# Kernel tuning notes

Hardware: AMD Instinct MI355X
Metric: run time of the kernel (lower is better)

## Reference

```python
import jax, jax.numpy as jnp
import numpy as np

B, S, D, E, K = 4, 2048, 1024, 8, 2
EPS, W_THRES, TEMP = 1e-4, 0.1, 1.0


def setup_inputs() -> dict:
    key = jax.random.key(0)
    k1, k2, k3, k4, k5 = jax.random.split(key, 5)
    x = jax.random.normal(k1, (B, S, D), dtype=jnp.float32)
    gate_W = jax.random.normal(k2, (D, E), dtype=jnp.float32) * 0.02
    gate_b = jnp.zeros((E,), dtype=jnp.float32)
    expert_W = jax.random.normal(k3, (E, D, D), dtype=jnp.float32) * 0.02
    expert_b = jnp.zeros((E, D), dtype=jnp.float32)
    return {"x": x, "gate_W": gate_W, "gate_b": gate_b,
            "expert_W": expert_W, "expert_b": expert_b}


def reference(x, gate_W, gate_b, expert_W, expert_b):
    # Gating: linear -> temperature -> clamp-min(eps) -> softmax
    scores = jnp.maximum((x @ gate_W + gate_b) / TEMP, EPS)      # [B,S,E]
    p = jax.nn.softmax(scores, axis=-1)                           # [B,S,E]
    _, topk_idx = jax.lax.top_k(p, K)                             # [B,S,K]
    # boolean membership mask of selected experts
    topk_mask = jax.nn.one_hot(topk_idx, E, dtype=p.dtype).sum(-2) > 0  # [B,S,E]
    # weights: clamp-min(weight_thres), normalized by detached sum over selected
    w = jnp.maximum(p, W_THRES)                                   # [B,S,E]
    w_gather = jnp.take_along_axis(w, topk_idx, axis=-1)          # [B,S,K]
    total = jax.lax.stop_gradient(w_gather.sum(-1, keepdims=True))
    w = w / total
    comb = jnp.where(topk_mask, w, jnp.zeros_like(w))             # [B,S,E]
    # Dense equivalent of gather/expert/scatter loop (E small): each expert
    # is Linear(D, D); masked combine weights zero out unselected experts.
    y = jnp.einsum('bsd,edf->bsef', x, expert_W) + expert_b       # [B,S,E,D]
    out = jnp.einsum('bsef,bse->bsf', y, comb) / K                # [B,S,D]
    return out
```

## Files before the change

kernel.cpp:

```cpp
#include <hip/hip_runtime.h>
#include <stdint.h>

#define TOK 8192
#define DIM 1024
#define NE 8
#define NTILE 136

typedef short bf16x8 __attribute__((ext_vector_type(8)));
typedef float f32x4 __attribute__((ext_vector_type(4)));

__device__ __forceinline__ unsigned short f2bf(float f) {
  unsigned int u = __float_as_uint(f);
  u += 0x7FFFu + ((u >> 16) & 1u);
  return (unsigned short)(u >> 16);
}

__device__ __forceinline__ void gl_lds16(const void* g, void* l) {
  __builtin_amdgcn_global_load_lds(
      (__attribute__((address_space(1))) unsigned int*)(g),
      (__attribute__((address_space(3))) unsigned int*)(l), 16, 0, 0);
}

__global__ __launch_bounds__(256) void gate_kernel(
    const float* __restrict__ x, const float* __restrict__ gW,
    const float* __restrict__ gb, unsigned short* __restrict__ xb,
    int* __restrict__ eSel, float* __restrict__ wSel, int* __restrict__ cnt)
{
  if (blockIdx.x == 0 && threadIdx.x < NE) cnt[threadIdx.x] = 0;

  const int wave = threadIdx.x >> 6;
  const int lane = threadIdx.x & 63;
  const int t = blockIdx.x * 4 + wave;
  const float4* xrow = (const float4*)(x + (size_t)t * DIM);
  ushort4* xbrow = (ushort4*)(xb + (size_t)t * DIM);

  double acc[NE];
#pragma unroll
  for (int e = 0; e < NE; ++e) acc[e] = 0.0;

#pragma unroll
  for (int i = 0; i < 4; ++i) {
    const int j = i * 64 + lane;
    float4 v = xrow[j];
    ushort4 pk;
    pk.x = f2bf(v.x); pk.y = f2bf(v.y); pk.z = f2bf(v.z); pk.w = f2bf(v.w);
    xbrow[j] = pk;
    const float* g = gW + (size_t)j * 4 * NE;
    float xv[4] = {v.x, v.y, v.z, v.w};
#pragma unroll
    for (int c = 0; c < 4; ++c) {
#pragma unroll
      for (int e = 0; e < NE; ++e)
        acc[e] += (double)xv[c] * (double)g[c * NE + e];
    }
  }
#pragma unroll
  for (int off = 32; off > 0; off >>= 1) {
#pragma unroll
    for (int e = 0; e < NE; ++e)
      acc[e] += __shfl_xor(acc[e], off, 64);
  }

  if (lane == 0) {
    double s[NE];
#pragma unroll
    for (int e = 0; e < NE; ++e) {
      s[e] = acc[e] + (double)gb[e];
      if (s[e] < 1e-4) s[e] = 1e-4;
    }
    int e0 = 0;
    for (int e = 1; e < NE; ++e) if (s[e] > s[e0]) e0 = e;
    int e1 = (e0 == 0) ? 1 : 0;
    for (int e = 0; e < NE; ++e) if (e != e0 && s[e] > s[e1]) e1 = e;
    float m = (float)s[e0];
    float Z = 0.f, pf[NE];
#pragma unroll
    for (int e = 0; e < NE; ++e) { pf[e] = __expf((float)s[e] - m); Z += pf[e]; }
    float w0 = pf[e0] / Z; if (w0 < 0.1f) w0 = 0.1f;
    float w1 = pf[e1] / Z; if (w1 < 0.1f) w1 = 0.1f;
    const float inv = 0.5f / (w0 + w1);
    eSel[t * 2 + 0] = e0;
    eSel[t * 2 + 1] = e1;
    wSel[t * 2 + 0] = w0 * inv;
    wSel[t * 2 + 1] = w1 * inv;
  }
}

__global__ __launch_bounds__(256) void scatter_kernel(
    const int* __restrict__ eSel, const float* __restrict__ wSel,
    int* __restrict__ cnt, int* __restrict__ listTok, float* __restrict__ listW)
{
  __shared__ int lcnt[NE];
  __shared__ int base[NE];
  const int tid = threadIdx.x;
  if (tid < NE) lcnt[tid] = 0;
  __syncthreads();

  const int t = blockIdx.x * 256 + tid;
  const int e0 = eSel[t * 2 + 0];
  const int e1 = eSel[t * 2 + 1];
  const float w0 = wSel[t * 2 + 0];
  const float w1 = wSel[t * 2 + 1];
  const int l0 = atomicAdd(&lcnt[e0], 1);
  const int l1 = atomicAdd(&lcnt[e1], 1);
  __syncthreads();
  if (tid < NE) base[tid] = atomicAdd(&cnt[tid], lcnt[tid]);
  __syncthreads();

  const int p0 = base[e0] + l0;
  listTok[e0 * TOK + p0] = t * 2 + 0;
  listW [e0 * TOK + p0] = w0;
  const int p1 = base[e1] + l1;
  listTok[e1 * TOK + p1] = t * 2 + 1;
  listW [e1 * TOK + p1] = w1;
}

__global__ __launch_bounds__(256) void transpose_w(
    const float* __restrict__ W, unsigned short* __restrict__ Wt)
{
  __shared__ float t[32 * 17 + 16];
  const int e  = blockIdx.x >> 6;
  const int fb = blockIdx.x & 63;
  const int f0 = fb * 16;
  const int tid = threadIdx.x;
  const float* Wb = W + (size_t)e * DIM * DIM + f0;
  unsigned short* Ob = Wt + ((size_t)(e * 64 + fb) * 32) * 512;

  for (int kc = 0; kc < 32; ++kc) {
    const int d0 = kc * 32;
    __syncthreads();
#pragma unroll
    for (int h = 0; h < 512; h += 256) {
      const int idx = tid + h;
      t[(idx >> 4) * 17 + (idx & 15)] = Wb[(size_t)(d0 + (idx >> 4)) * DIM + (idx & 15)];
    }
    __syncthreads();
#pragma unroll
    for (int h = 0; h < 512; h += 256) {
      const int o = tid + h;
      Ob[(size_t)kc * 512 + o] = f2bf(t[(o & 31) * 17 + (o >> 5)]);
    }
  }
}

__global__ __launch_bounds__(256) void moe_gemm(
    const unsigned short* __restrict__ xb, const unsigned short* __restrict__ Wt,
    const float* __restrict__ eb, const int* __restrict__ cnt,
    const int* __restrict__ listTok, const float* __restrict__ listW,
    float* __restrict__ yslot)
{
  const int dId = blockIdx.x % NTILE;
  const int cT  = blockIdx.x / NTILE;
  int e = -1, r0 = 0, rows = 0, accT = 0;
#pragma unroll
  for (int ee = 0; ee < NE; ++ee) {
    const int c = cnt[ee];
    const int nt = (c + 127) >> 7;
    if (dId >= accT && dId < accT + nt) {
      e = ee; r0 = (dId - accT) * 128;
      rows = c - r0; if (rows > 128) rows = 128;
    }
    accT += nt;
  }
  if (e < 0) return;

  __shared__ __align__(16) unsigned short As[2][128 * 32];
  __shared__ int   tid_s[128];
  __shared__ float w_s[128];

  const int tid = threadIdx.x;
  if (tid < 128) {
    if (tid < rows) {
      tid_s[tid] = listTok[e * TOK + r0 + tid];
      w_s[tid]   = listW [e * TOK + r0 + tid];
    } else {
      tid_s[tid] = 0;
      w_s[tid]   = 0.0f;
    }
  }
  __syncthreads();

  const int w    = tid >> 6;
  const int lane = tid & 63;
  const int qsrc = (lane & 3) ^ ((lane >> 3) & 3);
  const int rA0  = w * 32 + (lane >> 2);
  const int rA1  = rA0 + 16;
  const unsigned short* srcA0 = xb + (size_t)(tid_s[rA0] >> 1) * DIM + qsrc * 8;
  const unsigned short* srcA1 = xb + (size_t)(tid_s[rA1] >> 1) * DIM + qsrc * 8;

  const int wr = w >> 1, wc = w & 1;
  const int mrow = lane & 15;
  const int qg   = lane >> 4;
  const int qsA  = (qg ^ ((mrow >> 1) & 3)) * 8;

  const unsigned short* bbase =
      Wt + ((size_t)(e * 64 + cT * 8 + wc * 4) * 32) * 512 + mrow * 32 + qg * 8;

  f32x4 acc[4][4];
#pragma unroll
  for (int i = 0; i < 4; ++i)
#pragma unroll
    for (int j = 0; j < 4; ++j)
      acc[i][j] = {0.f, 0.f, 0.f, 0.f};

  gl_lds16(srcA0, &As[0][w * 1024]);
  gl_lds16(srcA1, &As[0][w * 1024 + 512]);

  for (int kc = 0; kc < DIM / 32; ++kc) {
    const int cur = kc & 1;
    __syncthreads();
    bf16x8 b[4];
#pragma unroll
    for (int nt = 0; nt < 4; ++nt)
      b[nt] = *(const bf16x8*)(bbase + (size_t)nt * 16384 + kc * 512);
    if (kc < DIM / 32 - 1) {
      const int k1 = (kc + 1) * 32;
      unsigned short* a = &As[cur ^ 1][w * 1024];
      gl_lds16(srcA0 + k1, a);
      gl_lds16(srcA1 + k1, a + 512);
    }
    bf16x8 af[4];
#pragma unroll
    for (int mt = 0; mt < 4; ++mt)
      af[mt] = *(const bf16x8*)&As[cur][(wr * 64 + mt * 16 + mrow) * 32 + qsA];
#pragma unroll
    for (int nt = 0; nt < 4; ++nt)
#pragma unroll
      for (int mt = 0; mt < 4; ++mt)
        acc[mt][nt] = __builtin_amdgcn_mfma_f32_16x16x32_bf16(
            af[mt], b[nt], acc[mt][nt], 0, 0, 0);
  }

  const int colBase = cT * 128 + wc * 64 + mrow;
  float bias[4];
#pragma unroll
  for (int nt = 0; nt < 4; ++nt)
    bias[nt] = eb[(size_t)e * DIM + colBase + nt * 16];
#pragma unroll
  for (int mt = 0; mt < 4; ++mt) {
#pragma unroll
    for (int r = 0; r < 4; ++r) {
      const int rloc = wr * 64 + mt * 16 + (lane >> 4) * 4 + r;
      if (rloc < rows) {
        const int tk    = tid_s[rloc];
        const float wgt = w_s[rloc];
        float* dst = yslot + ((size_t)(tk & 1) * TOK + (size_t)(tk >> 1)) * DIM;
#pragma unroll
        for (int nt = 0; nt < 4; ++nt)
          dst[colBase + nt * 16] = wgt * (acc[mt][nt][r] + bias[nt]);
      }
    }
  }
}

__global__ __launch_bounds__(256) void combine(
    const float4* __restrict__ y0, const float4* __restrict__ y1,
    float4* __restrict__ out)
{
  const size_t i = (size_t)blockIdx.x * 256 + threadIdx.x;
  float4 a = y0[i], b = y1[i];
  float4 o;
  o.x = a.x + b.x; o.y = a.y + b.y; o.z = a.z + b.z; o.w = a.w + b.w;
  out[i] = o;
}

extern "C" void kernel_launch(void* const* d_in, const int* in_sizes, int n_in,
                              void* d_out, int out_size, void* d_ws, size_t ws_size,
                              hipStream_t stream)
{
  const float* x  = (const float*)d_in[0];
  const float* gW = (const float*)d_in[1];
  const float* gb = (const float*)d_in[2];
  const float* eW = (const float*)d_in[3];
  const float* eb = (const float*)d_in[4];
  float* out = (float*)d_out;

  char* p = (char*)d_ws;
  unsigned short* xb = (unsigned short*)p;  p += (size_t)TOK * DIM * 2;
  unsigned short* Wt = (unsigned short*)p;  p += (size_t)NE * DIM * DIM * 2;
  float* yslot = (float*)p;                 p += (size_t)2 * TOK * DIM * 4;
  int* cnt = (int*)p;                       p += 256;
  int* listTok = (int*)p;                   p += (size_t)NE * TOK * 4;
  float* listW = (float*)p;                 p += (size_t)NE * TOK * 4;

  int*   eSel = (int*)yslot;
  float* wSel = (float*)(yslot + TOK * 2);

  gate_kernel<<<TOK / 4, 256, 0, stream>>>(x, gW, gb, xb, eSel, wSel, cnt);
  scatter_kernel<<<TOK / 256, 256, 0, stream>>>(eSel, wSel, cnt, listTok, listW);
  transpose_w<<<NE * 64, 256, 0, stream>>>(eW, Wt);
  moe_gemm<<<NTILE * 8, 256, 0, stream>>>(xb, Wt, eb, cnt, listTok, listW, yslot);
  combine<<<TOK * DIM / 4 / 256, 256, 0, stream>>>(
      (const float4*)yslot, (const float4*)yslot + (size_t)TOK * DIM / 4, (float4*)out);
}
```

Before: 233.2 us.

## Stage gate weights in LDS, stage B tiles via LDS, store expert outputs in fp16

The gate kernel now copies the gate weights into shared memory once per block in an expert-major layout, replacing the strided global loads in its dot products. The expert weight transpose now writes a plain row-major [f][d] bf16 layout. The GEMM streams B tiles into double-buffered LDS with async global-to-LDS loads, the same way it already handles A, instead of loading B fragments straight from global memory per step. Per-slot expert outputs are written as fp16, which halves the intermediate write and read traffic in the combine step but adds rounding error and extra LDS use per block.

```diff
diff --git a/kernel.cpp b/kernel.cpp
--- a/kernel.cpp
+++ b/kernel.cpp
@@ -1,4 +1,5 @@
 #include <hip/hip_runtime.h>
+#include <hip/hip_fp16.h>
 #include <stdint.h>
 
 #define TOK 8192
@@ -27,6 +28,19 @@
     int* __restrict__ eSel, float* __restrict__ wSel, int* __restrict__ cnt)
 {
   if (blockIdx.x == 0 && threadIdx.x < NE) cnt[threadIdx.x] = 0;
+
+  __shared__ float gWs[NE * DIM];
+#pragma unroll
+  for (int h = 0; h < 8; ++h) {
+    const int m = threadIdx.x + h * 256;
+    float4 v = ((const float4*)gW)[m];
+    const int d = m >> 1, e0 = (m & 1) * 4;
+    gWs[(e0 + 0) * DIM + d] = v.x;
+    gWs[(e0 + 1) * DIM + d] = v.y;
+    gWs[(e0 + 2) * DIM + d] = v.z;
+    gWs[(e0 + 3) * DIM + d] = v.w;
+  }
+  __syncthreads();
 
   const int wave = threadIdx.x >> 6;
   const int lane = threadIdx.x & 63;
@@ -45,13 +59,11 @@
     ushort4 pk;
     pk.x = f2bf(v.x); pk.y = f2bf(v.y); pk.z = f2bf(v.z); pk.w = f2bf(v.w);
     xbrow[j] = pk;
-    const float* g = gW + (size_t)j * 4 * NE;
-    float xv[4] = {v.x, v.y, v.z, v.w};
-#pragma unroll
-    for (int c = 0; c < 4; ++c) {
-#pragma unroll
-      for (int e = 0; e < NE; ++e)
-        acc[e] += (double)xv[c] * (double)g[c * NE + e];
+#pragma unroll
+    for (int e = 0; e < NE; ++e) {
+      float4 gv = *(const float4*)&gWs[e * DIM + j * 4];
+      acc[e] += (double)v.x * (double)gv.x + (double)v.y * (double)gv.y
+              + (double)v.z * (double)gv.z + (double)v.w * (double)gv.w;
     }
   }
 #pragma unroll
@@ -118,27 +130,27 @@
 __global__ __launch_bounds__(256) void transpose_w(
     const float* __restrict__ W, unsigned short* __restrict__ Wt)
 {
-  __shared__ float t[32 * 17 + 16];
-  const int e  = blockIdx.x >> 6;
-  const int fb = blockIdx.x & 63;
-  const int f0 = fb * 16;
+  __shared__ float t2[64 * 33];
+  const int e  = blockIdx.x >> 5;
+  const int fb = blockIdx.x & 31;
+  const int f0 = fb * 32;
   const int tid = threadIdx.x;
   const float* Wb = W + (size_t)e * DIM * DIM + f0;
-  unsigned short* Ob = Wt + ((size_t)(e * 64 + fb) * 32) * 512;
-
-  for (int kc = 0; kc < 32; ++kc) {
-    const int d0 = kc * 32;
+  unsigned short* Ob = Wt + ((size_t)e * DIM + f0) * DIM;
+
+  for (int kc = 0; kc < 16; ++kc) {
+    const int d0 = kc * 64;
     __syncthreads();
 #pragma unroll
-    for (int h = 0; h < 512; h += 256) {
-      const int idx = tid + h;
-      t[(idx >> 4) * 17 + (idx & 15)] = Wb[(size_t)(d0 + (idx >> 4)) * DIM + (idx & 15)];
+    for (int h = 0; h < 8; ++h) {
+      const int idx = tid + h * 256;
+      t2[(idx >> 5) * 33 + (idx & 31)] = Wb[(size_t)(d0 + (idx >> 5)) * DIM + (idx & 31)];
     }
     __syncthreads();
 #pragma unroll
-    for (int h = 0; h < 512; h += 256) {
-      const int o = tid + h;
-      Ob[(size_t)kc * 512 + o] = f2bf(t[(o & 31) * 17 + (o >> 5)]);
+    for (int h = 0; h < 8; ++h) {
+      const int o = tid + h * 256;
+      Ob[(size_t)(o >> 6) * DIM + d0 + (o & 63)] = f2bf(t2[(o & 63) * 33 + (o >> 6)]);
     }
   }
 }
@@ -147,7 +159,7 @@
     const unsigned short* __restrict__ xb, const unsigned short* __restrict__ Wt,
     const float* __restrict__ eb, const int* __restrict__ cnt,
     const int* __restrict__ listTok, const float* __restrict__ listW,
-    float* __restrict__ yslot)
+    __half* __restrict__ yslot)
 {
   const int dId = blockIdx.x % NTILE;
   const int cT  = blockIdx.x / NTILE;
@@ -165,6 +177,7 @@
   if (e < 0) return;
 
   __shared__ __align__(16) unsigned short As[2][128 * 32];
+  __shared__ __align__(16) unsigned short Bs[2][128 * 32];
   __shared__ int   tid_s[128];
   __shared__ float w_s[128];
 
@@ -187,15 +200,14 @@
   const int rA1  = rA0 + 16;
   const unsigned short* srcA0 = xb + (size_t)(tid_s[rA0] >> 1) * DIM + qsrc * 8;
   const unsigned short* srcA1 = xb + (size_t)(tid_s[rA1] >> 1) * DIM + qsrc * 8;
+  const unsigned short* srcB0 = Wt + ((size_t)e * DIM + cT * 128 + rA0) * DIM + qsrc * 8;
+  const unsigned short* srcB1 = Wt + ((size_t)e * DIM + cT * 128 + rA1) * DIM + qsrc * 8;
 
   const int wr = w >> 1, wc = w & 1;
   const int mrow = lane & 15;
   const int qg   = lane >> 4;
   const int qsA  = (qg ^ ((mrow >> 1) & 3)) * 8;
 
-  const unsigned short* bbase =
-      Wt + ((size_t)(e * 64 + cT * 8 + wc * 4) * 32) * 512 + mrow * 32 + qg * 8;
-
   f32x4 acc[4][4];
 #pragma unroll
   for (int i = 0; i < 4; ++i)
@@ -205,30 +217,35 @@
 
   gl_lds16(srcA0, &As[0][w * 1024]);
   gl_lds16(srcA1, &As[0][w * 1024 + 512]);
-
+  gl_lds16(srcB0, &Bs[0][w * 1024]);
+  gl_lds16(srcB1, &Bs[0][w * 1024 + 512]);
+
+#pragma unroll 2
   for (int kc = 0; kc < DIM / 32; ++kc) {
     const int cur = kc & 1;
     __syncthreads();
-    bf16x8 b[4];
-#pragma unroll
-    for (int nt = 0; nt < 4; ++nt)
-      b[nt] = *(const bf16x8*)(bbase + (size_t)nt * 16384 + kc * 512);
     if (kc < DIM / 32 - 1) {
       const int k1 = (kc + 1) * 32;
       unsigned short* a = &As[cur ^ 1][w * 1024];
+      unsigned short* b = &Bs[cur ^ 1][w * 1024];
       gl_lds16(srcA0 + k1, a);
       gl_lds16(srcA1 + k1, a + 512);
-    }
-    bf16x8 af[4];
+      gl_lds16(srcB0 + k1, b);
+      gl_lds16(srcB1 + k1, b + 512);
+    }
+    bf16x8 af[4], bfr[4];
 #pragma unroll
     for (int mt = 0; mt < 4; ++mt)
       af[mt] = *(const bf16x8*)&As[cur][(wr * 64 + mt * 16 + mrow) * 32 + qsA];
 #pragma unroll
     for (int nt = 0; nt < 4; ++nt)
-#pragma unroll
-      for (int mt = 0; mt < 4; ++mt)
+      bfr[nt] = *(const bf16x8*)&Bs[cur][(wc * 64 + nt * 16 + mrow) * 32 + qsA];
+#pragma unroll
+    for (int mt = 0; mt < 4; ++mt)
+#pragma unroll
+      for (int nt = 0; nt < 4; ++nt)
         acc[mt][nt] = __builtin_amdgcn_mfma_f32_16x16x32_bf16(
-            af[mt], b[nt], acc[mt][nt], 0, 0, 0);
+            af[mt], bfr[nt], acc[mt][nt], 0, 0, 0);
   }
 
   const int colBase = cT * 128 + wc * 64 + mrow;
@@ -244,23 +261,29 @@
       if (rloc < rows) {
         const int tk    = tid_s[rloc];
         const float wgt = w_s[rloc];
-        float* dst = yslot + ((size_t)(tk & 1) * TOK + (size_t)(tk >> 1)) * DIM;
+        __half* dst = yslot + ((size_t)(tk & 1) * TOK + (size_t)(tk >> 1)) * DIM;
 #pragma unroll
         for (int nt = 0; nt < 4; ++nt)
-          dst[colBase + nt * 16] = wgt * (acc[mt][nt][r] + bias[nt]);
+          dst[colBase + nt * 16] = __float2half(wgt * (acc[mt][nt][r] + bias[nt]));
       }
     }
   }
 }
 
 __global__ __launch_bounds__(256) void combine(
-    const float4* __restrict__ y0, const float4* __restrict__ y1,
+    const __half* __restrict__ y0, const __half* __restrict__ y1,
     float4* __restrict__ out)
 {
   const size_t i = (size_t)blockIdx.x * 256 + threadIdx.x;
-  float4 a = y0[i], b = y1[i];
+  const ushort4 ua = ((const ushort4*)y0)[i];
+  const ushort4 ub = ((const ushort4*)y1)[i];
+  const __half* ah = (const __half*)&ua;
+  const __half* bh = (const __half*)&ub;
   float4 o;
-  o.x = a.x + b.x; o.y = a.y + b.y; o.z = a.z + b.z; o.w = a.w + b.w;
+  o.x = __half2float(ah[0]) + __half2float(bh[0]);
+  o.y = __half2float(ah[1]) + __half2float(bh[1]);
+  o.z = __half2float(ah[2]) + __half2float(bh[2]);
+  o.w = __half2float(ah[3]) + __half2float(bh[3]);
   out[i] = o;
 }
 
@@ -278,18 +301,18 @@
   char* p = (char*)d_ws;
   unsigned short* xb = (unsigned short*)p;  p += (size_t)TOK * DIM * 2;
   unsigned short* Wt = (unsigned short*)p;  p += (size_t)NE * DIM * DIM * 2;
-  float* yslot = (float*)p;                 p += (size_t)2 * TOK * DIM * 4;
+  __half* yslot = (__half*)p;               p += (size_t)2 * TOK * DIM * 2;
   int* cnt = (int*)p;                       p += 256;
   int* listTok = (int*)p;                   p += (size_t)NE * TOK * 4;
   float* listW = (float*)p;                 p += (size_t)NE * TOK * 4;
 
   int*   eSel = (int*)yslot;
-  float* wSel = (float*)(yslot + TOK * 2);
+  float* wSel = (float*)((char*)yslot + TOK * 8);
 
   gate_kernel<<<TOK / 4, 256, 0, stream>>>(x, gW, gb, xb, eSel, wSel, cnt);
   scatter_kernel<<<TOK / 256, 256, 0, stream>>>(eSel, wSel, cnt, listTok, listW);
-  transpose_w<<<NE * 64, 256, 0, stream>>>(eW, Wt);
+  transpose_w<<<NE * 32, 256, 0, stream>>>(eW, Wt);
   moe_gemm<<<NTILE * 8, 256, 0, stream>>>(xb, Wt, eb, cnt, listTok, listW, yslot);
   combine<<<TOK * DIM / 4 / 256, 256, 0, stream>>>(
-      (const float4*)yslot, (const float4*)yslot + (size_t)TOK * DIM / 4, (float4*)out);
-}
+      yslot, yslot + (size_t)TOK * DIM, (float4*)out);
+}
```

New measurement: 214.0 us. 1.09x faster.
